# Performance work log

Hardware: AMD Instinct MI355X
Metric: run time of the kernel (lower is better)

## Reference

```python
import jax, jax.numpy as jnp
import numpy as np

# dims
B, T, H = 4, 2048, 768
HEADS, D = 4, 768          # GATConv(out_channels=768, heads=4, concat=False)
L = 3                      # num_layers
WIN = 2
K = 2 * WIN + 1
EPS = 1e-5
NEG_SLOPE = 0.2            # PyG GATConv leaky_relu slope


def setup_inputs() -> dict:
    key = jax.random.key(0)
    ks = jax.random.split(key, 4)
    s = 1.0 / np.sqrt(H)
    x = jax.random.normal(ks[0], (B, T, H), jnp.float32)
    W = jax.random.normal(ks[1], (L, H, HEADS, D), jnp.float32) * s   # lin weights per layer
    a_src = jax.random.normal(ks[2], (L, HEADS, D), jnp.float32) * s  # att_src
    a_dst = jax.random.normal(ks[3], (L, HEADS, D), jnp.float32) * s  # att_dst
    bias = jnp.zeros((L, D), jnp.float32)                             # GATConv bias (concat=False -> [D])
    gamma = jnp.ones((L, H), jnp.float32)                             # LayerNorm weight
    beta = jnp.zeros((L, H), jnp.float32)                             # LayerNorm bias
    return {"x": x, "W": W, "a_src": a_src, "a_dst": a_dst,
            "bias": bias, "gamma": gamma, "beta": beta}


def _layernorm(z, g, b):
    m = jnp.mean(z, axis=-1, keepdims=True)
    v = jnp.mean((z - m) ** 2, axis=-1, keepdims=True)
    return (z - m) * jax.lax.rsqrt(v + EPS) * g + b


def _gat_layer(x, Wl, asrc_w, adst_w, bias_l, idx, mask):
    # x: [B,T,H]; banded GAT with neighborhoods idx: [T,K] (clipped), mask: [T,K]
    h = jnp.einsum('bti,ihd->bthd', x, Wl)                 # [B,T,heads,D]
    asrc = jnp.einsum('bthd,hd->bth', h, asrc_w)           # per-source-node score term
    adst = jnp.einsum('bthd,hd->bth', h, adst_w)           # per-target-node score term
    h_nb = h[:, idx]                                       # [B,T,K,heads,D] gathered neighbors j
    score = jax.nn.leaky_relu(asrc[:, idx] + adst[:, :, None, :], NEG_SLOPE)  # [B,T,K,heads]
    score = jnp.where(mask[None, :, :, None], score, -jnp.inf)
    attn = jax.nn.softmax(score, axis=2)                   # softmax over incoming edges per target
    out = jnp.einsum('btkh,btkhd->bthd', attn, h_nb)       # weighted aggregation
    return out.mean(axis=2) + bias_l                       # concat=False -> mean over heads


def reference(x, W, a_src, a_dst, bias, gamma, beta):
    # banded neighborhood indices (window edges both directions + self-loop from PyG default)
    offs = jnp.arange(-WIN, WIN + 1)
    idx = jnp.arange(T)[:, None] + offs[None, :]           # [T,K]
    mask = (idx >= 0) & (idx < T)
    idx = jnp.clip(idx, 0, T - 1)
    for l in range(L):
        res = x
        y = _gat_layer(x, W[l], a_src[l], a_dst[l], bias[l], idx, mask)
        x = _layernorm(y + res, gamma[l], beta[l])         # dropout = identity in eval
    return x
```

## Files before the change

kernel.cpp:

```cpp
#include <hip/hip_runtime.h>
#include <stdint.h>

#define TT 2048
#define BB 4
#define HH 768
#define NHEADS 4
#define DD 768
#define NN 3072
#define LL 3
#define BT 8192
#define KNB 5
#define NBLK 12

typedef __bf16 bf16x8 __attribute__((ext_vector_type(8)));
typedef float f32x4 __attribute__((ext_vector_type(4)));

__device__ __forceinline__ unsigned short f2bf(float f){
  union { float f; unsigned u; } v; v.f = f;
  unsigned u = v.u;
  return (unsigned short)((u + 0x7FFFu + ((u >> 16) & 1u)) >> 16);
}
__device__ __forceinline__ float bf2f(unsigned short h){
  union { unsigned u; float f; } v; v.u = ((unsigned)h) << 16;
  return v.f;
}
__device__ __forceinline__ void gload16(const unsigned short* g, unsigned short* l){
  __builtin_amdgcn_global_load_lds((const __attribute__((address_space(1))) void*)g,
                                   (__attribute__((address_space(3))) void*)l, 16, 0, 0);
}

__global__ void wt_kernel(const float* __restrict__ W, unsigned short* __restrict__ Wt){
  __shared__ float tile[32][33];
  int l = blockIdx.z;
  int n0 = blockIdx.x * 32, k0 = blockIdx.y * 32;
  int tx = threadIdx.x, ty = threadIdx.y;
  const float* Wl = W + (size_t)l * HH * NN;
  for (int r = 0; r < 4; r++)
    tile[ty + r*8][tx] = Wl[(size_t)(k0 + ty + r*8) * NN + n0 + tx];
  __syncthreads();
  unsigned short* Wtl = Wt + (size_t)l * NN * HH;
  for (int r = 0; r < 4; r++){
    int n = n0 + ty + r*8;
    Wtl[(size_t)n * HH + k0 + tx] = f2bf(tile[tx][ty + r*8]);
  }
}

__global__ void xconv_kernel(const float* __restrict__ x, unsigned short* __restrict__ xb){
  int i = blockIdx.x * blockDim.x + threadIdx.x;
  float4 v = ((const float4*)x)[i];
  ushort4 o;
  o.x = f2bf(v.x); o.y = f2bf(v.y); o.z = f2bf(v.z); o.w = f2bf(v.w);
  *(ushort4*)(xb + (size_t)i * 4) = o;
}

#define BM 128
#define BN 128
#define BK 64

__global__ __launch_bounds__(256, 3) void gemm_kernel(
    const unsigned short* __restrict__ xb,
    const unsigned short* __restrict__ wt,
    unsigned short* __restrict__ hout,
    const float* __restrict__ a_srcl,
    const float* __restrict__ a_dstl,
    float* __restrict__ psrc,
    float* __restrict__ pdst){
  __shared__ __align__(16) unsigned short xs[BM][BK];
  __shared__ __align__(16) unsigned short wsd[BN][BK];
  int id = blockIdx.x;
  int xcd = id & 7;
  int s = id >> 3;
  int bn_i = s / 8;
  int bm_i = (s & 7) + xcd * 8;
  int bm = bm_i * BM;
  int bn = bn_i * BN;
  int tid = threadIdx.x;
  int wave = tid >> 6, lane = tid & 63;
  int m16 = lane & 15, q = lane >> 4;
  int wm = (wave >> 1) * 64, wn = (wave & 1) * 64;
  int r8 = lane >> 3, c8 = lane & 7;
  int cg = (c8 ^ r8) * 8;
  const unsigned short* ga[4]; const unsigned short* gb[4];
  unsigned short* la[4]; unsigned short* lb[4];
  #pragma unroll
  for (int ss = 0; ss < 4; ss++){
    int row = wave * 32 + ss * 8;
    ga[ss] = xb + (size_t)(bm + row + r8) * HH + cg;
    gb[ss] = wt + (size_t)(bn + row + r8) * HH + cg;
    la[ss] = &xs[row][0];
    lb[ss] = &wsd[row][0];
  }
  int rd0 = ((0 + q) ^ (m16 & 7)) * 8;
  int rd1 = ((4 + q) ^ (m16 & 7)) * 8;
  f32x4 acc[4][4] = {};
  for (int k0 = 0; k0 < HH; k0 += BK){
    #pragma unroll
    for (int ss = 0; ss < 4; ss++){
      gload16(ga[ss] + k0, la[ss]);
      gload16(gb[ss] + k0, lb[ss]);
    }
    __syncthreads();
    bf16x8 af[4], bfr[4];
    for (int i = 0; i < 4; i++)
      af[i] = __builtin_bit_cast(bf16x8, *(const uint4*)(&xs[wm + i*16 + m16][rd0]));
    for (int j = 0; j < 4; j++)
      bfr[j] = __builtin_bit_cast(bf16x8, *(const uint4*)(&wsd[wn + j*16 + m16][rd0]));
    for (int i = 0; i < 4; i++)
      for (int j = 0; j < 4; j++)
        acc[i][j] = __builtin_amdgcn_mfma_f32_16x16x32_bf16(af[i], bfr[j], acc[i][j], 0, 0, 0);
    for (int i = 0; i < 4; i++)
      af[i] = __builtin_bit_cast(bf16x8, *(const uint4*)(&xs[wm + i*16 + m16][rd1]));
    for (int j = 0; j < 4; j++)
      bfr[j] = __builtin_bit_cast(bf16x8, *(const uint4*)(&wsd[wn + j*16 + m16][rd1]));
    for (int i = 0; i < 4; i++)
      for (int j = 0; j < 4; j++)
        acc[i][j] = __builtin_amdgcn_mfma_f32_16x16x32_bf16(af[i], bfr[j], acc[i][j], 0, 0, 0);
    __syncthreads();
  }
  for (int i = 0; i < 4; i++){
    int row0 = bm + wm + i*16 + q*4;
    for (int j = 0; j < 4; j++){
      int col = bn + wn + j*16 + m16;
      unsigned short* hp = hout + (size_t)row0 * NN + col;
      hp[0]            = f2bf(acc[i][j][0]);
      hp[NN]           = f2bf(acc[i][j][1]);
      hp[2*(size_t)NN] = f2bf(acc[i][j][2]);
      hp[3*(size_t)NN] = f2bf(acc[i][j][3]);
    }
  }
  int col0 = bn + wn;
  int head = col0 / DD;
  int blk  = (col0 % DD) >> 6;
  float wsrc[4], wdstw[4];
  for (int j = 0; j < 4; j++){
    int n = col0 + j*16 + m16;
    wsrc[j]  = a_srcl[n];
    wdstw[j] = a_dstl[n];
  }
  for (int i = 0; i < 4; i++){
    for (int reg = 0; reg < 4; reg++){
      float ss = 0.f, dd = 0.f;
      for (int j = 0; j < 4; j++){
        float v = acc[i][j][reg];
        ss += v * wsrc[j];
        dd += v * wdstw[j];
      }
      ss += __shfl_xor(ss, 1, 64); dd += __shfl_xor(dd, 1, 64);
      ss += __shfl_xor(ss, 2, 64); dd += __shfl_xor(dd, 2, 64);
      ss += __shfl_xor(ss, 4, 64); dd += __shfl_xor(dd, 4, 64);
      ss += __shfl_xor(ss, 8, 64); dd += __shfl_xor(dd, 8, 64);
      if (m16 == 0){
        int row = bm + wm + i*16 + q*4 + reg;
        size_t slot = (size_t)row * (NHEADS * NBLK) + head * NBLK + blk;
        psrc[slot] = ss;
        pdst[slot] = dd;
      }
    }
  }
}

__global__ __launch_bounds__(512) void attn_ln_kernel(const unsigned short* __restrict__ h,
    const float* __restrict__ psrc, const float* __restrict__ pdst,
    const float* __restrict__ xin_f32,
    const unsigned short* __restrict__ xin_bf,
    const float* __restrict__ bias_l,
    const float* __restrict__ gamma_l, const float* __restrict__ beta_l,
    float* __restrict__ x_out, unsigned short* __restrict__ xb_next,
    int write_f32){
  int bid = blockIdx.x;
  int grp = ((bid & 7) << 7) | (bid >> 3);
  int wave = threadIdx.x >> 6, lane = threadIdx.x & 63;
  int token = grp * 8 + wave;
  int t = token & (TT - 1);
  int bseq = token >> 11;

  float red = 0.f;
  if (lane < 24){
    const float* p;
    if (lane < 20){
      int k = lane >> 2, hd = lane & 3;
      int row = min(max(t - 2 + k, 0), TT - 1);
      p = psrc + ((size_t)(bseq * TT + row) * NHEADS + hd) * NBLK;
    } else {
      int hd = lane - 20;
      p = pdst + ((size_t)(bseq * TT + t) * NHEADS + hd) * NBLK;
    }
    float4 a = *(const float4*)(p);
    float4 b = *(const float4*)(p + 4);
    float4 d = *(const float4*)(p + 8);
    red = a.x+a.y+a.z+a.w + b.x+b.y+b.z+b.w + d.x+d.y+d.z+d.w;
  }

  const unsigned short* hb = h + (size_t)(bseq * TT) * NN + lane * 4;
  float y[12] = {};
  #pragma unroll
  for (int hd = 0; hd < NHEADS; hd++){
    float ad = __shfl(red, 20 + hd, 64);
    float sc[KNB];
    float mx = -3.0e38f;
    #pragma unroll
    for (int k = 0; k < KNB; k++){
      int tn = t + k - 2;
      if (tn >= 0 && tn < TT){
        float s = __shfl(red, k * 4 + hd, 64) + ad;
        s = s > 0.f ? s : 0.2f * s;
        sc[k] = s; mx = fmaxf(mx, s);
      } else sc[k] = -3.0e38f;
    }
    float den = 0.f;
    #pragma unroll
    for (int k = 0; k < KNB; k++){
      float e = (sc[k] > -1.0e38f) ? __expf(sc[k] - mx) : 0.f;
      sc[k] = e; den += e;
    }
    float inv = 0.25f / den;
    #pragma unroll
    for (int k = 0; k < KNB; k++){
      int g = t + k - 2;
      g = min(max(g, 0), TT - 1);
      const unsigned short* hr = hb + (size_t)g * NN + hd * DD;
      float a = sc[k] * inv;
      #pragma unroll
      for (int j = 0; j < 3; j++){
        uint2 u = *(const uint2*)(hr + j * 256);
        const unsigned short* us = (const unsigned short*)&u;
        y[j*4+0] += a * bf2f(us[0]);
        y[j*4+1] += a * bf2f(us[1]);
        y[j*4+2] += a * bf2f(us[2]);
        y[j*4+3] += a * bf2f(us[3]);
      }
    }
  }

  float xr[12], bb[12];
  if (xin_f32){
    const float* xp = xin_f32 + (size_t)token * HH + lane * 4;
    #pragma unroll
    for (int j = 0; j < 3; j++) *(float4*)&xr[j*4] = *(const float4*)(xp + j * 256);
  } else {
    const unsigned short* xp = xin_bf + (size_t)token * HH + lane * 4;
    #pragma unroll
    for (int j = 0; j < 3; j++){
      uint2 u = *(const uint2*)(xp + j * 256);
      const unsigned short* us = (const unsigned short*)&u;
      xr[j*4+0] = bf2f(us[0]); xr[j*4+1] = bf2f(us[1]);
      xr[j*4+2] = bf2f(us[2]); xr[j*4+3] = bf2f(us[3]);
    }
  }
  { const float* p = bias_l + lane * 4;
    #pragma unroll
    for (int j = 0; j < 3; j++) *(float4*)&bb[j*4] = *(const float4*)(p + j * 256); }
  float s = 0.f, sq = 0.f;
  #pragma unroll
  for (int e = 0; e < 12; e++){
    float zz = y[e] + bb[e] + xr[e];
    y[e] = zz; s += zz; sq += zz * zz;
  }
  #pragma unroll
  for (int off = 32; off > 0; off >>= 1){
    s  += __shfl_xor(s, off, 64);
    sq += __shfl_xor(sq, off, 64);
  }
  float mean = s * (1.f / HH);
  float var = sq * (1.f / HH) - mean * mean;
  float rstd = rsqrtf(var + 1e-5f);

  float gr[12], br[12];
  { const float* p = gamma_l + lane * 4;
    #pragma unroll
    for (int j = 0; j < 3; j++) *(float4*)&gr[j*4] = *(const float4*)(p + j * 256); }
  { const float* p = beta_l + lane * 4;
    #pragma unroll
    for (int j = 0; j < 3; j++) *(float4*)&br[j*4] = *(const float4*)(p + j * 256); }

  float o[12];
  #pragma unroll
  for (int e = 0; e < 12; e++)
    o[e] = (y[e] - mean) * rstd * gr[e] + br[e];

  if (write_f32){
    float* xo = x_out + (size_t)token * HH + lane * 4;
    #pragma unroll
    for (int j = 0; j < 3; j++) *(float4*)(xo + j * 256) = *(float4*)&o[j*4];
  } else {
    unsigned short* xo = xb_next + (size_t)token * HH + lane * 4;
    #pragma unroll
    for (int j = 0; j < 3; j++){
      ushort4 o16;
      o16.x = f2bf(o[j*4+0]); o16.y = f2bf(o[j*4+1]);
      o16.z = f2bf(o[j*4+2]); o16.w = f2bf(o[j*4+3]);
      *(ushort4*)(xo + j * 256) = o16;
    }
  }
}

extern "C" void kernel_launch(void* const* d_in, const int* in_sizes, int n_in,
                              void* d_out, int out_size, void* d_ws, size_t ws_size,
                              hipStream_t stream) {
  const float* x     = (const float*)d_in[0];
  const float* W     = (const float*)d_in[1];
  const float* a_src = (const float*)d_in[2];
  const float* a_dst = (const float*)d_in[3];
  const float* bias  = (const float*)d_in[4];
  const float* gamma = (const float*)d_in[5];
  const float* beta  = (const float*)d_in[6];
  float* out = (float*)d_out;

  char* ws = (char*)d_ws;
  size_t off = 0;
  auto alloc = [&](size_t bytes)->char*{
    char* p = ws + off;
    off = (off + bytes + 255) & ~(size_t)255;
    return p;
  };
  unsigned short* wt   = (unsigned short*)alloc((size_t)LL * NN * HH * 2);
  unsigned short* xb   = (unsigned short*)alloc((size_t)BT * HH * 2);
  unsigned short* hbuf = (unsigned short*)alloc((size_t)BT * NN * 2);
  float* psrc  = (float*)alloc((size_t)BT * NHEADS * NBLK * 4);
  float* pdst  = (float*)alloc((size_t)BT * NHEADS * NBLK * 4);

  wt_kernel<<<dim3(NN/32, HH/32, LL), dim3(32, 8), 0, stream>>>(W, wt);
  xconv_kernel<<<(BT * HH / 4) / 256, 256, 0, stream>>>(x, xb);

  for (int l = 0; l < LL; l++){
    gemm_kernel<<<(NN / BN) * (BT / BM), 256, 0, stream>>>(
        xb, wt + (size_t)l * NN * HH, hbuf,
        a_src + (size_t)l * NHEADS * DD, a_dst + (size_t)l * NHEADS * DD,
        psrc, pdst);
    attn_ln_kernel<<<BT / 8, 512, 0, stream>>>(hbuf, psrc, pdst,
        (l == 0) ? x : nullptr, xb,
        bias + (size_t)l * DD, gamma + (size_t)l * HH, beta + (size_t)l * HH,
        out, xb, (l == LL - 1) ? 1 : 0);
  }
}
```

Before: 324.6 us.

## Prepack weights into MFMA fragment layout and load B operands directly from global

The weight conversion kernel now writes bf16 weights pre-swizzled into the per-lane MFMA B-fragment order, so each lane fetches its B operand with one 16-byte global load. The GEMM no longer stages B through LDS, which halves shared-memory use and LDS traffic per k-step and may raise occupancy. In exchange, B fragments come straight from global/L2 with no reuse across waves in the block, so the two waves sharing a column tile each load it separately, and the loads are only partly hidden by the barrier.

```diff
diff --git a/kernel.cpp b/kernel.cpp
--- a/kernel.cpp
+++ b/kernel.cpp
@@ -11,6 +11,7 @@
 #define BT 8192
 #define KNB 5
 #define NBLK 12
+#define NKT 12
 
 typedef __bf16 bf16x8 __attribute__((ext_vector_type(8)));
 typedef float f32x4 __attribute__((ext_vector_type(4)));
@@ -28,21 +29,32 @@
   __builtin_amdgcn_global_load_lds((const __attribute__((address_space(1))) void*)g,
                                    (__attribute__((address_space(3))) void*)l, 16, 0, 0);
 }
-
-__global__ void wt_kernel(const float* __restrict__ W, unsigned short* __restrict__ Wt){
-  __shared__ float tile[32][33];
-  int l = blockIdx.z;
-  int n0 = blockIdx.x * 32, k0 = blockIdx.y * 32;
-  int tx = threadIdx.x, ty = threadIdx.y;
+__device__ __forceinline__ bf16x8 ld16(const unsigned short* p){
+  return __builtin_bit_cast(bf16x8, *(const uint4*)p);
+}
+
+__global__ void wtf_kernel(const float* __restrict__ W, unsigned short* __restrict__ wtf){
+  __shared__ float lds[64][17];
+  int n16 = blockIdx.x, kt = blockIdx.y, l = blockIdx.z;
+  int t = threadIdx.x;
   const float* Wl = W + (size_t)l * HH * NN;
-  for (int r = 0; r < 4; r++)
-    tile[ty + r*8][tx] = Wl[(size_t)(k0 + ty + r*8) * NN + n0 + tx];
+  {
+    int r = t >> 2, cg = t & 3;
+    float4 v = *(const float4*)(Wl + (size_t)(kt*64 + r) * NN + n16*16 + cg*4);
+    lds[r][cg*4+0] = v.x; lds[r][cg*4+1] = v.y;
+    lds[r][cg*4+2] = v.z; lds[r][cg*4+3] = v.w;
+  }
   __syncthreads();
-  unsigned short* Wtl = Wt + (size_t)l * NN * HH;
-  for (int r = 0; r < 4; r++){
-    int n = n0 + ty + r*8;
-    Wtl[(size_t)n * HH + k0 + tx] = f2bf(tile[tx][ty + r*8]);
-  }
+  int ks = t >> 7, L = (t >> 1) & 63, eh = (t & 1) * 4;
+  int m16 = L & 15, q = L >> 4;
+  ushort4 o;
+  o.x = f2bf(lds[ks*32 + q*8 + eh + 0][m16]);
+  o.y = f2bf(lds[ks*32 + q*8 + eh + 1][m16]);
+  o.z = f2bf(lds[ks*32 + q*8 + eh + 2][m16]);
+  o.w = f2bf(lds[ks*32 + q*8 + eh + 3][m16]);
+  unsigned short* out = wtf + (size_t)l * NN * HH +
+      ((size_t)(n16 * NKT + kt) * 2 + ks) * 512 + L * 8 + eh;
+  *(ushort4*)out = o;
 }
 
 __global__ void xconv_kernel(const float* __restrict__ x, unsigned short* __restrict__ xb){
@@ -59,14 +71,13 @@
 
 __global__ __launch_bounds__(256, 3) void gemm_kernel(
     const unsigned short* __restrict__ xb,
-    const unsigned short* __restrict__ wt,
+    const unsigned short* __restrict__ wtf,
     unsigned short* __restrict__ hout,
     const float* __restrict__ a_srcl,
     const float* __restrict__ a_dstl,
     float* __restrict__ psrc,
     float* __restrict__ pdst){
   __shared__ __align__(16) unsigned short xs[BM][BK];
-  __shared__ __align__(16) unsigned short wsd[BN][BK];
   int id = blockIdx.x;
   int xcd = id & 7;
   int s = id >> 3;
@@ -80,41 +91,49 @@
   int wm = (wave >> 1) * 64, wn = (wave & 1) * 64;
   int r8 = lane >> 3, c8 = lane & 7;
   int cg = (c8 ^ r8) * 8;
-  const unsigned short* ga[4]; const unsigned short* gb[4];
-  unsigned short* la[4]; unsigned short* lb[4];
+  const unsigned short* ga[4];
+  unsigned short* la[4];
   #pragma unroll
   for (int ss = 0; ss < 4; ss++){
     int row = wave * 32 + ss * 8;
     ga[ss] = xb + (size_t)(bm + row + r8) * HH + cg;
-    gb[ss] = wt + (size_t)(bn + row + r8) * HH + cg;
     la[ss] = &xs[row][0];
-    lb[ss] = &wsd[row][0];
-  }
+  }
+  const unsigned short* bj[4];
+  #pragma unroll
+  for (int j = 0; j < 4; j++)
+    bj[j] = wtf + (size_t)(((bn + wn) >> 4) + j) * NKT * 1024 + lane * 8;
   int rd0 = ((0 + q) ^ (m16 & 7)) * 8;
   int rd1 = ((4 + q) ^ (m16 & 7)) * 8;
   f32x4 acc[4][4] = {};
-  for (int k0 = 0; k0 < HH; k0 += BK){
-    #pragma unroll
-    for (int ss = 0; ss < 4; ss++){
+  for (int kt = 0; kt < NKT; kt++){
+    int k0 = kt * BK;
+    #pragma unroll
+    for (int ss = 0; ss < 4; ss++)
       gload16(ga[ss] + k0, la[ss]);
-      gload16(gb[ss] + k0, lb[ss]);
-    }
+    bf16x8 b0[4], b1[4];
+    #pragma unroll
+    for (int j = 0; j < 4; j++) b0[j] = ld16(bj[j] + kt*1024);
+    #pragma unroll
+    for (int j = 0; j < 4; j++) b1[j] = ld16(bj[j] + kt*1024 + 512);
     __syncthreads();
-    bf16x8 af[4], bfr[4];
+    bf16x8 af[4];
+    #pragma unroll
     for (int i = 0; i < 4; i++)
-      af[i] = __builtin_bit_cast(bf16x8, *(const uint4*)(&xs[wm + i*16 + m16][rd0]));
-    for (int j = 0; j < 4; j++)
-      bfr[j] = __builtin_bit_cast(bf16x8, *(const uint4*)(&wsd[wn + j*16 + m16][rd0]));
+      af[i] = ld16(&xs[wm + i*16 + m16][rd0]);
+    #pragma unroll
     for (int i = 0; i < 4; i++)
+      #pragma unroll
       for (int j = 0; j < 4; j++)
-        acc[i][j] = __builtin_amdgcn_mfma_f32_16x16x32_bf16(af[i], bfr[j], acc[i][j], 0, 0, 0);
+        acc[i][j] = __builtin_amdgcn_mfma_f32_16x16x32_bf16(af[i], b0[j], acc[i][j], 0, 0, 0);
+    #pragma unroll
     for (int i = 0; i < 4; i++)
-      af[i] = __builtin_bit_cast(bf16x8, *(const uint4*)(&xs[wm + i*16 + m16][rd1]));
-    for (int j = 0; j < 4; j++)
-      bfr[j] = __builtin_bit_cast(bf16x8, *(const uint4*)(&wsd[wn + j*16 + m16][rd1]));
+      af[i] = ld16(&xs[wm + i*16 + m16][rd1]);
+    #pragma unroll
     for (int i = 0; i < 4; i++)
+      #pragma unroll
       for (int j = 0; j < 4; j++)
-        acc[i][j] = __builtin_amdgcn_mfma_f32_16x16x32_bf16(af[i], bfr[j], acc[i][j], 0, 0, 0);
+        acc[i][j] = __builtin_amdgcn_mfma_f32_16x16x32_bf16(af[i], b1[j], acc[i][j], 0, 0, 0);
     __syncthreads();
   }
   for (int i = 0; i < 4; i++){
@@ -313,18 +332,18 @@
     off = (off + bytes + 255) & ~(size_t)255;
     return p;
   };
-  unsigned short* wt   = (unsigned short*)alloc((size_t)LL * NN * HH * 2);
+  unsigned short* wtf  = (unsigned short*)alloc((size_t)LL * NN * HH * 2);
   unsigned short* xb   = (unsigned short*)alloc((size_t)BT * HH * 2);
   unsigned short* hbuf = (unsigned short*)alloc((size_t)BT * NN * 2);
   float* psrc  = (float*)alloc((size_t)BT * NHEADS * NBLK * 4);
   float* pdst  = (float*)alloc((size_t)BT * NHEADS * NBLK * 4);
 
-  wt_kernel<<<dim3(NN/32, HH/32, LL), dim3(32, 8), 0, stream>>>(W, wt);
+  wtf_kernel<<<dim3(NN/16, NKT, LL), 256, 0, stream>>>(W, wtf);
   xconv_kernel<<<(BT * HH / 4) / 256, 256, 0, stream>>>(x, xb);
 
   for (int l = 0; l < LL; l++){
     gemm_kernel<<<(NN / BN) * (BT / BM), 256, 0, stream>>>(
-        xb, wt + (size_t)l * NN * HH, hbuf,
+        xb, wtf + (size_t)l * NN * HH, hbuf,
         a_src + (size_t)l * NHEADS * DD, a_dst + (size_t)l * NHEADS * DD,
         psrc, pdst);
     attn_ln_kernel<<<BT / 8, 512, 0, stream>>>(hbuf, psrc, pdst,
```

Measured after the change: 367.0 us. +13.1%, slower.
